# Performance work log

Measured on AMD Instinct MI355X. Metric: run time of the kernel, lower is better.

The kernel has to match this reference:

```python
import jax, jax.numpy as jnp
import numpy as np

EMBED = 256
HEADS = 8
GROUP = 64
HEAD_DIM = EMBED // HEADS
N = 131072

def setup_inputs() -> dict:
    key = jax.random.key(0)
    k1, k2, k3 = jax.random.split(key, 3)
    s_in = 1.0 / np.sqrt(EMBED)
    x = jax.random.normal(k1, (N, EMBED), dtype=jnp.float32)
    w_qkv = jax.random.normal(k2, (3 * EMBED, EMBED), dtype=jnp.float32) * s_in  # nn.Linear weight [out,in]
    w_out = jax.random.normal(k3, (EMBED, EMBED), dtype=jnp.float32) * s_in
    b_out = jnp.zeros((EMBED,), dtype=jnp.float32)
    return {"x": x, "w_qkv": w_qkv, "w_out": w_out, "b_out": b_out}

def reference(x, w_qkv, w_out, b_out):
    Ntok, C = x.shape
    ng = Ntok // GROUP  # number of groups
    qkv = x @ w_qkv.T                      # (N, 3C)
    qkv = qkv.reshape(Ntok, 3, C)
    q, k, v = qkv[:, 0], qkv[:, 1], qkv[:, 2]

    def to_heads(t):
        # '(n g) (h c) -> (n h) g c'
        t = t.reshape(ng, GROUP, HEADS, HEAD_DIM)
        return t.transpose(0, 2, 1, 3).reshape(ng * HEADS, GROUP, HEAD_DIM)

    q, k, v = to_heads(q), to_heads(k), to_heads(v)
    # grouped attention over local windows of size GROUP
    energy = jnp.einsum('nqd,nkd->nqk', q, k)           # (n*h, g, g)
    attn = jax.nn.softmax(energy / jnp.sqrt(jnp.float32(C)), axis=-1)  # scale by sqrt(embed_size), as in source
    out = jnp.einsum('nql,nld->nqd', attn, v)           # (n*h, g, hd)
    # '(n h) g c -> (n g) (h c)'
    out = out.reshape(ng, HEADS, GROUP, HEAD_DIM).transpose(0, 2, 1, 3).reshape(Ntok, C)
    return out @ w_out.T + b_out
```

## Files before the change

### kernel.cpp

```cpp
#include <hip/hip_runtime.h>
#include <hip/hip_bf16.h>
#include <stdint.h>

typedef __attribute__((ext_vector_type(8))) short s16x8;
typedef __attribute__((ext_vector_type(4))) float f32x4;

__device__ __forceinline__ unsigned short f32_bf16(float f) {
  union { float f; uint32_t u; } v; v.f = f;
  return (unsigned short)((v.u + 0x7FFFu + ((v.u >> 16) & 1u)) >> 16);
}

__device__ __forceinline__ uint32_t pack_bf16(float lo, float hi) {
  __hip_bfloat162 h = __float22bfloat162_rn(float2{lo, hi});
  union { __hip_bfloat162 h; uint32_t u; } u; u.h = h; return u.u;
}

__device__ __forceinline__ s16x8 xchg(uint32_t lo0, uint32_t lo1,
                                      uint32_t hi0, uint32_t hi1,
                                      int srcA, int srcB, uint32_t hisel) {
  int a0 = __shfl((int)lo0, srcA), b0 = __shfl((int)hi0, srcA);
  int a1 = __shfl((int)lo1, srcA), b1 = __shfl((int)hi1, srcA);
  int a2 = __shfl((int)lo0, srcB), b2 = __shfl((int)hi0, srcB);
  int a3 = __shfl((int)lo1, srcB), b3 = __shfl((int)hi1, srcB);
  union { uint32_t u[4]; s16x8 v; } r;
  r.u[0] = hisel ? (uint32_t)b0 : (uint32_t)a0;
  r.u[1] = hisel ? (uint32_t)b1 : (uint32_t)a1;
  r.u[2] = hisel ? (uint32_t)b2 : (uint32_t)a2;
  r.u[3] = hisel ? (uint32_t)b3 : (uint32_t)a3;
  return r.v;
}

__global__ void convert_w(const float* __restrict__ wqkv,
                          const float* __restrict__ wout,
                          unsigned short* __restrict__ o) {
  int i = blockIdx.x * 256 + threadIdx.x;
  if (i < 768 * 256) o[i] = f32_bf16(wqkv[i]);
  else               o[i] = f32_bf16(wout[i - 768 * 256]);
}

__global__ __launch_bounds__(256, 2) void mha_fused(
    const float* __restrict__ x,
    const unsigned short* __restrict__ wqkv,
    const unsigned short* __restrict__ wout,
    const float* __restrict__ bias,
    float* __restrict__ out) {
  __shared__ unsigned short xt[64 * 256];
  __shared__ unsigned short ot0[64 * 128];

  const int g    = blockIdx.x;
  const int tid  = threadIdx.x;
  const int w    = tid >> 6;
  const int lane = tid & 63;
  const int l15  = lane & 15;
  const int l4   = lane >> 4;

  {
    const int rr = tid >> 5;
    const int cc = (tid & 31) * 8;
#pragma unroll
    for (int it = 0; it < 8; ++it) {
      int row = rr + 8 * it;
      const float* src = x + (size_t)(g * 64 + row) * 256 + cc;
      float4 f0 = *(const float4*)(src);
      float4 f1 = *(const float4*)(src + 4);
      uint32_t p0 = pack_bf16(f0.x, f0.y);
      uint32_t p1 = pack_bf16(f0.z, f0.w);
      uint32_t p2 = pack_bf16(f1.x, f1.y);
      uint32_t p3 = pack_bf16(f1.z, f1.w);
      uint32_t byte = ((uint32_t)(row * 512 + cc * 2)) ^ ((uint32_t)(row & 7) << 4);
      *(uint4*)((char*)xt + byte) = make_uint4(p0, p1, p2, p3);
    }
  }
  __syncthreads();

  const uint32_t swz   = (uint32_t)(l15 & 7) << 4;
  const int      srcA  = l15 + ((lane & 16) << 1);
  const int      srcB  = srcA + 16;
  const uint32_t hisel = (uint32_t)(lane & 32);

#pragma unroll 1
  for (int hh = 0; hh < 2; ++hh) {
    const int h = w + 4 * hh;
    const unsigned short* wbase = wqkv + (size_t)(h * 32 + l15) * 256 + l4 * 8;

    s16x8 qB[4], kA[4];
    {
      f32x4 qT[2][4], kT[2][4];
#pragma unroll
      for (int t = 0; t < 2; ++t)
#pragma unroll
        for (int m = 0; m < 4; ++m) {
          qT[t][m] = (f32x4){0.f, 0.f, 0.f, 0.f};
          kT[t][m] = (f32x4){0.f, 0.f, 0.f, 0.f};
        }
      for (int kk = 0; kk < 8; ++kk) {
        s16x8 a[4];
#pragma unroll
        for (int m = 0; m < 4; ++m) {
          uint32_t byte = ((uint32_t)((16 * m + l15) * 512 + kk * 64 + l4 * 16)) ^ swz;
          a[m] = *(const s16x8*)((const char*)xt + byte);
        }
#pragma unroll
        for (int t = 0; t < 2; ++t) {
          s16x8 wq = *(const s16x8*)(wbase + (size_t)(16 * t) * 256 + kk * 32);
          s16x8 wk = *(const s16x8*)(wbase + (size_t)(256 + 16 * t) * 256 + kk * 32);
#pragma unroll
          for (int m = 0; m < 4; ++m) {
            qT[t][m] = __builtin_amdgcn_mfma_f32_16x16x32_bf16(wq, a[m], qT[t][m], 0, 0, 0);
            kT[t][m] = __builtin_amdgcn_mfma_f32_16x16x32_bf16(wk, a[m], kT[t][m], 0, 0, 0);
          }
        }
      }
#pragma unroll
      for (int m = 0; m < 4; ++m) {
        qB[m] = xchg(pack_bf16(qT[0][m][0], qT[0][m][1]), pack_bf16(qT[0][m][2], qT[0][m][3]),
                     pack_bf16(qT[1][m][0], qT[1][m][1]), pack_bf16(qT[1][m][2], qT[1][m][3]),
                     srcA, srcB, hisel);
        kA[m] = xchg(pack_bf16(kT[0][m][0], kT[0][m][1]), pack_bf16(kT[0][m][2], kT[0][m][3]),
                     pack_bf16(kT[1][m][0], kT[1][m][1]), pack_bf16(kT[1][m][2], kT[1][m][3]),
                     srcA, srcB, hisel);
      }
    }

    s16x8 vB[2][2];
    {
      f32x4 vv[4][2];
#pragma unroll
      for (int m = 0; m < 4; ++m) {
        vv[m][0] = (f32x4){0.f, 0.f, 0.f, 0.f};
        vv[m][1] = (f32x4){0.f, 0.f, 0.f, 0.f};
      }
      for (int kk = 0; kk < 8; ++kk) {
        s16x8 a[4];
#pragma unroll
        for (int m = 0; m < 4; ++m) {
          uint32_t byte = ((uint32_t)((16 * m + l15) * 512 + kk * 64 + l4 * 16)) ^ swz;
          a[m] = *(const s16x8*)((const char*)xt + byte);
        }
        const unsigned short* wp = wbase + (size_t)512 * 256 + kk * 32;
        s16x8 wv0 = *(const s16x8*)(wp);
        s16x8 wv1 = *(const s16x8*)(wp + 16 * 256);
#pragma unroll
        for (int m = 0; m < 4; ++m) {
          vv[m][0] = __builtin_amdgcn_mfma_f32_16x16x32_bf16(a[m], wv0, vv[m][0], 0, 0, 0);
          vv[m][1] = __builtin_amdgcn_mfma_f32_16x16x32_bf16(a[m], wv1, vv[m][1], 0, 0, 0);
        }
      }
      uint32_t pkv[2][4][2];
#pragma unroll
      for (int t = 0; t < 2; ++t)
#pragma unroll
        for (int m = 0; m < 4; ++m) {
          pkv[t][m][0] = pack_bf16(vv[m][t][0], vv[m][t][1]);
          pkv[t][m][1] = pack_bf16(vv[m][t][2], vv[m][t][3]);
        }
#pragma unroll
      for (int kk2 = 0; kk2 < 2; ++kk2)
#pragma unroll
        for (int t = 0; t < 2; ++t)
          vB[kk2][t] = xchg(pkv[t][2 * kk2][0], pkv[t][2 * kk2][1],
                            pkv[t][2 * kk2 + 1][0], pkv[t][2 * kk2 + 1][1],
                            srcA, srcB, hisel);
    }

    if (hh == 1) __syncthreads();

#pragma unroll
    for (int nb = 0; nb < 4; ++nb) {
      f32x4 en[4];
#pragma unroll
      for (int m = 0; m < 4; ++m) {
        en[m] = (f32x4){0.f, 0.f, 0.f, 0.f};
        en[m] = __builtin_amdgcn_mfma_f32_16x16x32_bf16(kA[m], qB[nb], en[m], 0, 0, 0);
      }
      float mx = en[0][0];
#pragma unroll
      for (int m = 0; m < 4; ++m)
#pragma unroll
        for (int r = 0; r < 4; ++r) mx = fmaxf(mx, en[m][r]);
      mx = fmaxf(mx, __shfl_xor(mx, 16));
      mx = fmaxf(mx, __shfl_xor(mx, 32));
      float p[4][4];
      float sum = 0.f;
#pragma unroll
      for (int m = 0; m < 4; ++m)
#pragma unroll
        for (int r = 0; r < 4; ++r) {
          float t = __expf((en[m][r] - mx) * 0.0625f);
          p[m][r] = t;
          sum += t;
        }
      sum += __shfl_xor(sum, 16);
      sum += __shfl_xor(sum, 32);
      float rs = 1.0f / sum;
      uint32_t pk[4][2];
#pragma unroll
      for (int m = 0; m < 4; ++m) {
        pk[m][0] = pack_bf16(p[m][0] * rs, p[m][1] * rs);
        pk[m][1] = pack_bf16(p[m][2] * rs, p[m][3] * rs);
      }
      f32x4 o0 = (f32x4){0.f, 0.f, 0.f, 0.f};
      f32x4 o1 = (f32x4){0.f, 0.f, 0.f, 0.f};
#pragma unroll
      for (int kk2 = 0; kk2 < 2; ++kk2) {
        s16x8 pA = xchg(pk[2 * kk2][0], pk[2 * kk2][1],
                        pk[2 * kk2 + 1][0], pk[2 * kk2 + 1][1], srcA, srcB, hisel);
        o0 = __builtin_amdgcn_mfma_f32_16x16x32_bf16(pA, vB[kk2][0], o0, 0, 0, 0);
        o1 = __builtin_amdgcn_mfma_f32_16x16x32_bf16(pA, vB[kk2][1], o1, 0, 0, 0);
      }
#pragma unroll
      for (int r = 0; r < 4; ++r) {
        int row = 16 * nb + 4 * l4 + r;
        uint32_t rsw = (uint32_t)(row & 7) << 4;
        if (hh == 0) {
          uint32_t b0 = ((uint32_t)(row * 256 + (w * 32 + l15) * 2)) ^ rsw;
          uint32_t b1 = ((uint32_t)(row * 256 + (w * 32 + 16 + l15) * 2)) ^ rsw;
          *(unsigned short*)((char*)ot0 + b0) = f32_bf16(o0[r]);
          *(unsigned short*)((char*)ot0 + b1) = f32_bf16(o1[r]);
        } else {
          uint32_t b0 = ((uint32_t)(row * 512 + (128 + w * 32 + l15) * 2)) ^ rsw;
          uint32_t b1 = ((uint32_t)(row * 512 + (128 + w * 32 + 16 + l15) * 2)) ^ rsw;
          *(unsigned short*)((char*)xt + b0) = f32_bf16(o0[r]);
          *(unsigned short*)((char*)xt + b1) = f32_bf16(o1[r]);
        }
      }
    }
  }
  __syncthreads();

#pragma unroll 1
  for (int pp = 0; pp < 2; ++pp) {
    const int colbase = 128 * pp + w * 32;
    const unsigned short* wobase = wout + (size_t)(colbase + l15) * 256 + l4 * 8;
    f32x4 acc[4][2];
#pragma unroll
    for (int m = 0; m < 4; ++m) {
      acc[m][0] = (f32x4){0.f, 0.f, 0.f, 0.f};
      acc[m][1] = (f32x4){0.f, 0.f, 0.f, 0.f};
    }
#pragma unroll
    for (int kk = 0; kk < 8; ++kk) {
      s16x8 a[4];
#pragma unroll
      for (int m = 0; m < 4; ++m) {
        int row = 16 * m + l15;
        if (kk < 4) {
          uint32_t byte = ((uint32_t)(row * 256 + kk * 64 + l4 * 16)) ^ swz;
          a[m] = *(const s16x8*)((const char*)ot0 + byte);
        } else {
          uint32_t byte = ((uint32_t)(row * 512 + kk * 64 + l4 * 16)) ^ swz;
          a[m] = *(const s16x8*)((const char*)xt + byte);
        }
      }
      s16x8 wo0 = *(const s16x8*)(wobase + kk * 32);
      s16x8 wo1 = *(const s16x8*)(wobase + (size_t)16 * 256 + kk * 32);
#pragma unroll
      for (int m = 0; m < 4; ++m) {
        acc[m][0] = __builtin_amdgcn_mfma_f32_16x16x32_bf16(a[m], wo0, acc[m][0], 0, 0, 0);
        acc[m][1] = __builtin_amdgcn_mfma_f32_16x16x32_bf16(a[m], wo1, acc[m][1], 0, 0, 0);
      }
    }
    const float b0 = bias[colbase + l15];
    const float b1 = bias[colbase + 16 + l15];
    float* dst = out + (size_t)g * 64 * 256 + colbase;
#pragma unroll
    for (int m = 0; m < 4; ++m)
#pragma unroll
      for (int r = 0; r < 4; ++r) {
        int tok = 16 * m + 4 * l4 + r;
        dst[(size_t)tok * 256 + l15]      = acc[m][0][r] + b0;
        dst[(size_t)tok * 256 + 16 + l15] = acc[m][1][r] + b1;
      }
  }
}

extern "C" void kernel_launch(void* const* d_in, const int* in_sizes, int n_in,
                              void* d_out, int out_size, void* d_ws, size_t ws_size,
                              hipStream_t stream) {
  const float* x    = (const float*)d_in[0];
  const float* wqkv = (const float*)d_in[1];
  const float* wout = (const float*)d_in[2];
  const float* bout = (const float*)d_in[3];
  float* out = (float*)d_out;

  unsigned short* wq_bf = (unsigned short*)d_ws;
  unsigned short* wo_bf = wq_bf + 768 * 256;

  convert_w<<<1024, 256, 0, stream>>>(wqkv, wout, wq_bf);
  mha_fused<<<2048, 256, 0, stream>>>(x, wq_bf, wo_bf, bout, out);
}
```

Before: 242.9 us.

## Split work across 16 waves per group with LDS-staged Q/K/V per head

Raises the block from 4 to 16 waves so each wave pair owns one head and handles half the token rows. Q, K and V are computed in one fused pass and staged through per-head LDS buffers, replacing the register shuffle exchanges. The output projection is split so each wave produces 16 columns. This adds parallelism and latency hiding within a block, at the cost of more LDS (about 128 KB per block), which limits how many blocks fit per CU, plus more barrier traffic.

```diff
diff --git a/kernel.cpp b/kernel.cpp
--- a/kernel.cpp
+++ b/kernel.cpp
@@ -38,14 +38,15 @@
   else               o[i] = f32_bf16(wout[i - 768 * 256]);
 }
 
-__global__ __launch_bounds__(256, 2) void mha_fused(
+__global__ __launch_bounds__(1024) void mha_fused(
     const float* __restrict__ x,
     const unsigned short* __restrict__ wqkv,
     const unsigned short* __restrict__ wout,
     const float* __restrict__ bias,
     float* __restrict__ out) {
   __shared__ unsigned short xt[64 * 256];
-  __shared__ unsigned short ot0[64 * 128];
+  __shared__ unsigned short qkb[8][64 * 64];
+  __shared__ unsigned short vtb[8][32 * 64];
 
   const int g    = blockIdx.x;
   const int tid  = threadIdx.x;
@@ -53,141 +54,144 @@
   const int lane = tid & 63;
   const int l15  = lane & 15;
   const int l4   = lane >> 4;
-
-  {
-    const int rr = tid >> 5;
-    const int cc = (tid & 31) * 8;
-#pragma unroll
-    for (int it = 0; it < 8; ++it) {
-      int row = rr + 8 * it;
-      const float* src = x + (size_t)(g * 64 + row) * 256 + cc;
-      float4 f0 = *(const float4*)(src);
-      float4 f1 = *(const float4*)(src + 4);
-      uint32_t p0 = pack_bf16(f0.x, f0.y);
-      uint32_t p1 = pack_bf16(f0.z, f0.w);
-      uint32_t p2 = pack_bf16(f1.x, f1.y);
-      uint32_t p3 = pack_bf16(f1.z, f1.w);
-      uint32_t byte = ((uint32_t)(row * 512 + cc * 2)) ^ ((uint32_t)(row & 7) << 4);
-      *(uint4*)((char*)xt + byte) = make_uint4(p0, p1, p2, p3);
-    }
+  const int h    = w >> 1;
+  const int s    = w & 1;
+
+  {
+    const int row = tid >> 4;
+    const int c0  = (tid & 15) * 16;
+    const float* src = x + (size_t)(g * 64 + row) * 256 + c0;
+    const uint32_t rsw = (uint32_t)(row & 7) << 4;
+    float4 f0 = *(const float4*)(src);
+    float4 f1 = *(const float4*)(src + 4);
+    float4 f2 = *(const float4*)(src + 8);
+    float4 f3 = *(const float4*)(src + 12);
+    uint32_t b0 = ((uint32_t)(row * 512 + c0 * 2)) ^ rsw;
+    uint32_t b1 = ((uint32_t)(row * 512 + c0 * 2 + 16)) ^ rsw;
+    *(uint4*)((char*)xt + b0) =
+        make_uint4(pack_bf16(f0.x, f0.y), pack_bf16(f0.z, f0.w),
+                   pack_bf16(f1.x, f1.y), pack_bf16(f1.z, f1.w));
+    *(uint4*)((char*)xt + b1) =
+        make_uint4(pack_bf16(f2.x, f2.y), pack_bf16(f2.z, f2.w),
+                   pack_bf16(f3.x, f3.y), pack_bf16(f3.z, f3.w));
   }
   __syncthreads();
 
-  const uint32_t swz   = (uint32_t)(l15 & 7) << 4;
+  const uint32_t xsw   = (uint32_t)(l15 & 7) << 4;
   const int      srcA  = l15 + ((lane & 16) << 1);
   const int      srcB  = srcA + 16;
   const uint32_t hisel = (uint32_t)(lane & 32);
 
-#pragma unroll 1
-  for (int hh = 0; hh < 2; ++hh) {
-    const int h = w + 4 * hh;
+  unsigned short* qkh = qkb[h];
+  unsigned short* vth = vtb[h];
+
+  {
+    f32x4 qT[2][2], kT[2][2], vv[2][2];
+#pragma unroll
+    for (int t = 0; t < 2; ++t)
+#pragma unroll
+      for (int m = 0; m < 2; ++m) {
+        qT[t][m] = (f32x4){0.f, 0.f, 0.f, 0.f};
+        kT[t][m] = (f32x4){0.f, 0.f, 0.f, 0.f};
+        vv[t][m] = (f32x4){0.f, 0.f, 0.f, 0.f};
+      }
     const unsigned short* wbase = wqkv + (size_t)(h * 32 + l15) * 256 + l4 * 8;
-
-    s16x8 qB[4], kA[4];
-    {
-      f32x4 qT[2][4], kT[2][4];
-#pragma unroll
-      for (int t = 0; t < 2; ++t)
-#pragma unroll
-        for (int m = 0; m < 4; ++m) {
-          qT[t][m] = (f32x4){0.f, 0.f, 0.f, 0.f};
-          kT[t][m] = (f32x4){0.f, 0.f, 0.f, 0.f};
+    for (int kk = 0; kk < 8; ++kk) {
+      s16x8 a[2];
+#pragma unroll
+      for (int m2 = 0; m2 < 2; ++m2) {
+        int tok = 16 * (2 * s + m2) + l15;
+        uint32_t byte = ((uint32_t)(tok * 512 + kk * 64 + l4 * 16)) ^ xsw;
+        a[m2] = *(const s16x8*)((const char*)xt + byte);
+      }
+#pragma unroll
+      for (int t = 0; t < 2; ++t) {
+        s16x8 wq = *(const s16x8*)(wbase + (size_t)(16 * t) * 256 + kk * 32);
+        s16x8 wk = *(const s16x8*)(wbase + (size_t)(256 + 16 * t) * 256 + kk * 32);
+        s16x8 wv = *(const s16x8*)(wbase + (size_t)(512 + 16 * t) * 256 + kk * 32);
+#pragma unroll
+        for (int m2 = 0; m2 < 2; ++m2) {
+          qT[t][m2] = __builtin_amdgcn_mfma_f32_16x16x32_bf16(wq, a[m2], qT[t][m2], 0, 0, 0);
+          kT[t][m2] = __builtin_amdgcn_mfma_f32_16x16x32_bf16(wk, a[m2], kT[t][m2], 0, 0, 0);
+          vv[t][m2] = __builtin_amdgcn_mfma_f32_16x16x32_bf16(a[m2], wv, vv[t][m2], 0, 0, 0);
         }
-      for (int kk = 0; kk < 8; ++kk) {
-        s16x8 a[4];
-#pragma unroll
-        for (int m = 0; m < 4; ++m) {
-          uint32_t byte = ((uint32_t)((16 * m + l15) * 512 + kk * 64 + l4 * 16)) ^ swz;
-          a[m] = *(const s16x8*)((const char*)xt + byte);
-        }
-#pragma unroll
-        for (int t = 0; t < 2; ++t) {
-          s16x8 wq = *(const s16x8*)(wbase + (size_t)(16 * t) * 256 + kk * 32);
-          s16x8 wk = *(const s16x8*)(wbase + (size_t)(256 + 16 * t) * 256 + kk * 32);
-#pragma unroll
-          for (int m = 0; m < 4; ++m) {
-            qT[t][m] = __builtin_amdgcn_mfma_f32_16x16x32_bf16(wq, a[m], qT[t][m], 0, 0, 0);
-            kT[t][m] = __builtin_amdgcn_mfma_f32_16x16x32_bf16(wk, a[m], kT[t][m], 0, 0, 0);
-          }
-        }
-      }
-#pragma unroll
-      for (int m = 0; m < 4; ++m) {
-        qB[m] = xchg(pack_bf16(qT[0][m][0], qT[0][m][1]), pack_bf16(qT[0][m][2], qT[0][m][3]),
-                     pack_bf16(qT[1][m][0], qT[1][m][1]), pack_bf16(qT[1][m][2], qT[1][m][3]),
-                     srcA, srcB, hisel);
-        kA[m] = xchg(pack_bf16(kT[0][m][0], kT[0][m][1]), pack_bf16(kT[0][m][2], kT[0][m][3]),
-                     pack_bf16(kT[1][m][0], kT[1][m][1]), pack_bf16(kT[1][m][2], kT[1][m][3]),
-                     srcA, srcB, hisel);
-      }
-    }
-
-    s16x8 vB[2][2];
-    {
-      f32x4 vv[4][2];
-#pragma unroll
-      for (int m = 0; m < 4; ++m) {
-        vv[m][0] = (f32x4){0.f, 0.f, 0.f, 0.f};
-        vv[m][1] = (f32x4){0.f, 0.f, 0.f, 0.f};
-      }
-      for (int kk = 0; kk < 8; ++kk) {
-        s16x8 a[4];
-#pragma unroll
-        for (int m = 0; m < 4; ++m) {
-          uint32_t byte = ((uint32_t)((16 * m + l15) * 512 + kk * 64 + l4 * 16)) ^ swz;
-          a[m] = *(const s16x8*)((const char*)xt + byte);
-        }
-        const unsigned short* wp = wbase + (size_t)512 * 256 + kk * 32;
-        s16x8 wv0 = *(const s16x8*)(wp);
-        s16x8 wv1 = *(const s16x8*)(wp + 16 * 256);
-#pragma unroll
-        for (int m = 0; m < 4; ++m) {
-          vv[m][0] = __builtin_amdgcn_mfma_f32_16x16x32_bf16(a[m], wv0, vv[m][0], 0, 0, 0);
-          vv[m][1] = __builtin_amdgcn_mfma_f32_16x16x32_bf16(a[m], wv1, vv[m][1], 0, 0, 0);
-        }
-      }
-      uint32_t pkv[2][4][2];
-#pragma unroll
-      for (int t = 0; t < 2; ++t)
-#pragma unroll
-        for (int m = 0; m < 4; ++m) {
-          pkv[t][m][0] = pack_bf16(vv[m][t][0], vv[m][t][1]);
-          pkv[t][m][1] = pack_bf16(vv[m][t][2], vv[m][t][3]);
-        }
-#pragma unroll
-      for (int kk2 = 0; kk2 < 2; ++kk2)
-#pragma unroll
-        for (int t = 0; t < 2; ++t)
-          vB[kk2][t] = xchg(pkv[t][2 * kk2][0], pkv[t][2 * kk2][1],
-                            pkv[t][2 * kk2 + 1][0], pkv[t][2 * kk2 + 1][1],
-                            srcA, srcB, hisel);
-    }
-
-    if (hh == 1) __syncthreads();
-
-#pragma unroll
-    for (int nb = 0; nb < 4; ++nb) {
+      }
+    }
+#pragma unroll
+    for (int t = 0; t < 2; ++t)
+#pragma unroll
+      for (int m2 = 0; m2 < 2; ++m2) {
+        int tok = 16 * (2 * s + m2) + l15;
+        uint32_t slq = (uint32_t)((2 * t + (l4 >> 1)) ^ (tok & 7)) << 4;
+        uint32_t slk = (uint32_t)((4 + 2 * t + (l4 >> 1)) ^ (tok & 7)) << 4;
+        uint32_t base = (uint32_t)(tok * 128) + (uint32_t)(l4 & 1) * 8;
+        *(uint2*)((char*)qkh + (base + slq)) =
+            make_uint2(pack_bf16(qT[t][m2][0], qT[t][m2][1]),
+                       pack_bf16(qT[t][m2][2], qT[t][m2][3]));
+        *(uint2*)((char*)qkh + (base + slk)) =
+            make_uint2(pack_bf16(kT[t][m2][0], kT[t][m2][1]),
+                       pack_bf16(kT[t][m2][2], kT[t][m2][3]));
+      }
+#pragma unroll
+    for (int t = 0; t < 2; ++t)
+#pragma unroll
+      for (int m2 = 0; m2 < 2; ++m2) {
+        int d = 16 * t + l15;
+        uint32_t sl = (uint32_t)((2 * (2 * s + m2) + (l4 >> 1)) ^ (d & 7)) << 4;
+        uint32_t byte = (uint32_t)(d * 128) + sl + (uint32_t)(l4 & 1) * 8;
+        *(uint2*)((char*)vth + byte) =
+            make_uint2(pack_bf16(vv[t][m2][0], vv[t][m2][1]),
+                       pack_bf16(vv[t][m2][2], vv[t][m2][3]));
+      }
+  }
+  __syncthreads();
+
+  {
+    s16x8 kA[4], qB[2], vB[2][2];
+#pragma unroll
+    for (int mb = 0; mb < 4; ++mb) {
+      int tok = 16 * mb + l15;
+      uint32_t byte = (uint32_t)(tok * 128) + ((uint32_t)((4 + l4) ^ (tok & 7)) << 4);
+      kA[mb] = *(const s16x8*)((const char*)qkh + byte);
+    }
+#pragma unroll
+    for (int nb = 0; nb < 2; ++nb) {
+      int tok = 16 * (2 * s + nb) + l15;
+      uint32_t byte = (uint32_t)(tok * 128) + ((uint32_t)(l4 ^ (tok & 7)) << 4);
+      qB[nb] = *(const s16x8*)((const char*)qkh + byte);
+    }
+#pragma unroll
+    for (int kk2 = 0; kk2 < 2; ++kk2)
+#pragma unroll
+      for (int t = 0; t < 2; ++t) {
+        int d = 16 * t + l15;
+        uint32_t byte = (uint32_t)(d * 128) + ((uint32_t)((4 * kk2 + l4) ^ (d & 7)) << 4);
+        vB[kk2][t] = *(const s16x8*)((const char*)vth + byte);
+      }
+
+#pragma unroll
+    for (int nb = 0; nb < 2; ++nb) {
       f32x4 en[4];
 #pragma unroll
-      for (int m = 0; m < 4; ++m) {
-        en[m] = (f32x4){0.f, 0.f, 0.f, 0.f};
-        en[m] = __builtin_amdgcn_mfma_f32_16x16x32_bf16(kA[m], qB[nb], en[m], 0, 0, 0);
+      for (int mb = 0; mb < 4; ++mb) {
+        en[mb] = (f32x4){0.f, 0.f, 0.f, 0.f};
+        en[mb] = __builtin_amdgcn_mfma_f32_16x16x32_bf16(kA[mb], qB[nb], en[mb], 0, 0, 0);
       }
       float mx = en[0][0];
 #pragma unroll
-      for (int m = 0; m < 4; ++m)
-#pragma unroll
-        for (int r = 0; r < 4; ++r) mx = fmaxf(mx, en[m][r]);
+      for (int mb = 0; mb < 4; ++mb)
+#pragma unroll
+        for (int r = 0; r < 4; ++r) mx = fmaxf(mx, en[mb][r]);
       mx = fmaxf(mx, __shfl_xor(mx, 16));
       mx = fmaxf(mx, __shfl_xor(mx, 32));
       float p[4][4];
       float sum = 0.f;
 #pragma unroll
-      for (int m = 0; m < 4; ++m)
+      for (int mb = 0; mb < 4; ++mb)
 #pragma unroll
         for (int r = 0; r < 4; ++r) {
-          float t = __expf((en[m][r] - mx) * 0.0625f);
-          p[m][r] = t;
+          float t = __expf((en[mb][r] - mx) * 0.0625f);
+          p[mb][r] = t;
           sum += t;
         }
       sum += __shfl_xor(sum, 16);
@@ -195,9 +199,9 @@
       float rs = 1.0f / sum;
       uint32_t pk[4][2];
 #pragma unroll
-      for (int m = 0; m < 4; ++m) {
-        pk[m][0] = pack_bf16(p[m][0] * rs, p[m][1] * rs);
-        pk[m][1] = pack_bf16(p[m][2] * rs, p[m][3] * rs);
+      for (int mb = 0; mb < 4; ++mb) {
+        pk[mb][0] = pack_bf16(p[mb][0] * rs, p[mb][1] * rs);
+        pk[mb][1] = pack_bf16(p[mb][2] * rs, p[mb][3] * rs);
       }
       f32x4 o0 = (f32x4){0.f, 0.f, 0.f, 0.f};
       f32x4 o1 = (f32x4){0.f, 0.f, 0.f, 0.f};
@@ -210,67 +214,43 @@
       }
 #pragma unroll
       for (int r = 0; r < 4; ++r) {
-        int row = 16 * nb + 4 * l4 + r;
+        int row = 16 * (2 * s + nb) + 4 * l4 + r;
         uint32_t rsw = (uint32_t)(row & 7) << 4;
-        if (hh == 0) {
-          uint32_t b0 = ((uint32_t)(row * 256 + (w * 32 + l15) * 2)) ^ rsw;
-          uint32_t b1 = ((uint32_t)(row * 256 + (w * 32 + 16 + l15) * 2)) ^ rsw;
-          *(unsigned short*)((char*)ot0 + b0) = f32_bf16(o0[r]);
-          *(unsigned short*)((char*)ot0 + b1) = f32_bf16(o1[r]);
-        } else {
-          uint32_t b0 = ((uint32_t)(row * 512 + (128 + w * 32 + l15) * 2)) ^ rsw;
-          uint32_t b1 = ((uint32_t)(row * 512 + (128 + w * 32 + 16 + l15) * 2)) ^ rsw;
-          *(unsigned short*)((char*)xt + b0) = f32_bf16(o0[r]);
-          *(unsigned short*)((char*)xt + b1) = f32_bf16(o1[r]);
-        }
+        uint32_t c0 = ((uint32_t)(row * 512 + (h * 32 + l15) * 2)) ^ rsw;
+        uint32_t c1 = ((uint32_t)(row * 512 + (h * 32 + 16 + l15) * 2)) ^ rsw;
+        *(unsigned short*)((char*)xt + c0) = f32_bf16(o0[r]);
+        *(unsigned short*)((char*)xt + c1) = f32_bf16(o1[r]);
       }
     }
   }
   __syncthreads();
 
-#pragma unroll 1
-  for (int pp = 0; pp < 2; ++pp) {
-    const int colbase = 128 * pp + w * 32;
+  {
+    const int colbase = w * 16;
     const unsigned short* wobase = wout + (size_t)(colbase + l15) * 256 + l4 * 8;
-    f32x4 acc[4][2];
-#pragma unroll
-    for (int m = 0; m < 4; ++m) {
-      acc[m][0] = (f32x4){0.f, 0.f, 0.f, 0.f};
-      acc[m][1] = (f32x4){0.f, 0.f, 0.f, 0.f};
-    }
+    f32x4 acc[4];
+#pragma unroll
+    for (int m = 0; m < 4; ++m) acc[m] = (f32x4){0.f, 0.f, 0.f, 0.f};
 #pragma unroll
     for (int kk = 0; kk < 8; ++kk) {
-      s16x8 a[4];
+      s16x8 a4[4];
 #pragma unroll
       for (int m = 0; m < 4; ++m) {
-        int row = 16 * m + l15;
-        if (kk < 4) {
-          uint32_t byte = ((uint32_t)(row * 256 + kk * 64 + l4 * 16)) ^ swz;
-          a[m] = *(const s16x8*)((const char*)ot0 + byte);
-        } else {
-          uint32_t byte = ((uint32_t)(row * 512 + kk * 64 + l4 * 16)) ^ swz;
-          a[m] = *(const s16x8*)((const char*)xt + byte);
-        }
-      }
-      s16x8 wo0 = *(const s16x8*)(wobase + kk * 32);
-      s16x8 wo1 = *(const s16x8*)(wobase + (size_t)16 * 256 + kk * 32);
-#pragma unroll
-      for (int m = 0; m < 4; ++m) {
-        acc[m][0] = __builtin_amdgcn_mfma_f32_16x16x32_bf16(a[m], wo0, acc[m][0], 0, 0, 0);
-        acc[m][1] = __builtin_amdgcn_mfma_f32_16x16x32_bf16(a[m], wo1, acc[m][1], 0, 0, 0);
-      }
-    }
-    const float b0 = bias[colbase + l15];
-    const float b1 = bias[colbase + 16 + l15];
-    float* dst = out + (size_t)g * 64 * 256 + colbase;
+        uint32_t byte = ((uint32_t)((16 * m + l15) * 512 + kk * 64 + l4 * 16)) ^ xsw;
+        a4[m] = *(const s16x8*)((const char*)xt + byte);
+      }
+      s16x8 wo = *(const s16x8*)(wobase + kk * 32);
+#pragma unroll
+      for (int m = 0; m < 4; ++m)
+        acc[m] = __builtin_amdgcn_mfma_f32_16x16x32_bf16(a4[m], wo, acc[m], 0, 0, 0);
+    }
+    const float b = bias[colbase + l15];
+    float* dst = out + (size_t)g * 64 * 256 + colbase + l15;
 #pragma unroll
     for (int m = 0; m < 4; ++m)
 #pragma unroll
-      for (int r = 0; r < 4; ++r) {
-        int tok = 16 * m + 4 * l4 + r;
-        dst[(size_t)tok * 256 + l15]      = acc[m][0][r] + b0;
-        dst[(size_t)tok * 256 + 16 + l15] = acc[m][1][r] + b1;
-      }
+      for (int r = 0; r < 4; ++r)
+        dst[(size_t)(16 * m + 4 * l4 + r) * 256] = acc[m][r] + b;
   }
 }
 
@@ -287,5 +267,5 @@
   unsigned short* wo_bf = wq_bf + 768 * 256;
 
   convert_w<<<1024, 256, 0, stream>>>(wqkv, wout, wq_bf);
-  mha_fused<<<2048, 256, 0, stream>>>(x, wq_bf, wo_bf, bout, out);
-}
+  mha_fused<<<2048, 1024, 0, stream>>>(x, wq_bf, wo_bf, bout, out);
+}
```

Result: slower. 269.7 us (+11.0%).
